# Kernel optimization log

Measured on AMD Instinct MI355X. Metric: run time of the kernel, lower is better.

The kernel has to match this reference:

```python
import jax, jax.numpy as jnp
import numpy as np

N_POINTS = 1048576
N_LEVELS = 16
F = 2
BASE_RES = 16
FINEST_RES = 512
LOG2_HASH = 19
SIZES = [2 ** min(i + 1, LOG2_HASH) for i in range(N_LEVELS)]  # per-level table rows (powers of 2)
OFFS = np.concatenate([[0], np.cumsum(SIZES)]).astype(np.int64)  # static row offsets into packed table
TOTAL_ROWS = int(OFFS[-1])  # 131070
# hash primes from the torch module; uint32 wraparound matches int64 low-bit behavior
# because each table size is a power of two <= 2^19 < 2^32, so h % 2^k == low k bits.
P0, P1, P2, P3 = np.uint32(1), np.uint32(2654435761), np.uint32(29675113), np.uint32(123456789)
CORNERS = np.array([[0,0,0],[1,0,0],[0,1,0],[1,1,0],
                    [0,0,1],[1,0,1],[0,1,1],[1,1,1]], dtype=np.uint32)  # torch stacking order


def setup_inputs() -> dict:
    key = jax.random.key(0)
    k1, k2 = jax.random.split(key)
    coords = jax.random.uniform(k1, (N_POINTS, 3), dtype=jnp.float32, minval=-1.0, maxval=1.0)
    hash_init_scale = 0.001
    table = jax.random.uniform(k2, (TOTAL_ROWS, F), dtype=jnp.float32,
                               minval=-hash_init_scale, maxval=hash_init_scale)
    return {"coords": coords, "table": table}


def _encode(coords, table):
    corners = jnp.asarray(CORNERS)  # [8,3] uint32
    outs = []
    for level in range(N_LEVELS):
        res = min(BASE_RES * (2 ** level), FINEST_RES)
        cs = (coords + 1.0) * res           # [N,3]
        cf = jnp.floor(cs)
        frac = cs - cf                      # [N,3]
        base = cf.astype(jnp.uint32)        # coords >= -1 so floor >= 0
        c = base[None, :, :] + corners[:, None, :]   # [8,N,3]
        x, y, z = c[..., 0], c[..., 1], c[..., 2]
        h = x * P0
        h = h * P1 + y
        h = h * P2 + z
        h = h * P3
        h = (h & jnp.uint32(SIZES[level] - 1)).astype(jnp.int32)  # mod power-of-2 table size
        feats = table[int(OFFS[level]) + h]          # [8,N,F] gather
        tx = frac[..., 0:1]; ty = frac[..., 1:2]; tz = frac[..., 2:3]
        f = (feats[0] * (1 - tx) * (1 - ty) * (1 - tz)
             + feats[1] * tx * (1 - ty) * (1 - tz)
             + feats[2] * (1 - tx) * ty * (1 - tz)
             + feats[3] * tx * ty * (1 - tz)
             + feats[4] * (1 - tx) * (1 - ty) * tz
             + feats[5] * tx * (1 - ty) * tz
             + feats[6] * (1 - tx) * ty * tz
             + feats[7] * tx * ty * tz)              # [N,F]
        outs.append(f)
    return jnp.concatenate(outs, axis=-1)            # [N, N_LEVELS*F]


def reference(coords, table):
    return _encode(coords, table)
```

## Files before the change

kernel.cpp:

```cpp
#include <hip/hip_runtime.h>
#include <hip/hip_fp16.h>


#define N_POINTS 1048576
#define BLOCK 1024
#define NBLOCKS 512
#define ITERS 16
#define STAGED_ROWS 16382
#define LDS_BYTES 65536

__device__ __forceinline__ float2 ldsRow(const unsigned* __restrict__ lds, unsigned idx) {
    unsigned u = lds[idx];
    __half2 h = *(__half2*)&u;
    return __half22float2(h);
}

__global__ __launch_bounds__(BLOCK) void ngp_encode_kernel(
    const float* __restrict__ coords,
    const float* __restrict__ table,
    float* __restrict__ out)
{
    extern __shared__ unsigned lds_tb[];

    {
        const float4* __restrict__ t4 = (const float4*)table;
        uint2* __restrict__ l2 = (uint2*)lds_tb;
        const int n = STAGED_ROWS / 2;
        for (int r = threadIdx.x; r < n; r += BLOCK) {
            float4 v = t4[r];
            __half2 a = __floats2half2_rn(v.x, v.y);
            __half2 b = __floats2half2_rn(v.z, v.w);
            uint2 u;
            u.x = *(unsigned*)&a;
            u.y = *(unsigned*)&b;
            l2[r] = u;
        }
    }
    __syncthreads();

    constexpr unsigned P1 = 2654435761u, P2 = 29675113u, P3 = 123456789u;
    constexpr unsigned HA = P1 * P2 * P3;
    constexpr unsigned HB = P2 * P3;
    constexpr unsigned HC = P3;
    const unsigned D[8] = {0u, HA, HB, HA + HB, HC, HA + HC, HB + HC, HA + HB + HC};

    const float2* __restrict__ tb = (const float2*)table;
    float4* __restrict__ out4 = (float4*)out;

    const int q = threadIdx.x & 7;

    for (int it = 0; it < ITERS; ++it) {
        const int t = (blockIdx.x * ITERS + it) * BLOCK + threadIdx.x;
        const int p = t >> 3;

        const float px = coords[3 * p + 0];
        const float py = coords[3 * p + 1];
        const float pz = coords[3 * p + 2];

        float4 result;
        float* rf = (float*)&result;

#pragma unroll
        for (int e = 0; e < 2; ++e) {
            const int l = 2 * q + e;
            const float fres = (l < 5) ? (float)(16 << l) : 512.0f;

            const float csx = (px + 1.0f) * fres;
            const float csy = (py + 1.0f) * fres;
            const float csz = (pz + 1.0f) * fres;
            const float cfx = floorf(csx), cfy = floorf(csy), cfz = floorf(csz);
            const float tx = csx - cfx, ty = csy - cfy, tz = csz - cfz;
            const unsigned h000 = (unsigned)cfx * HA + (unsigned)cfy * HB + (unsigned)cfz * HC;

            const float ux = 1.0f - tx, uy = 1.0f - ty, uz = 1.0f - tz;
            const float w[8] = {ux*uy*uz, tx*uy*uz, ux*ty*uz, tx*ty*uz,
                                ux*uy*tz, tx*uy*tz, ux*ty*tz, tx*ty*tz};

            const unsigned mask = (2u << l) - 1u;
            const unsigned off  = (2u << l) - 2u;

            float o0 = 0.0f, o1 = 0.0f;
            if (l <= 12) {
#pragma unroll
                for (int c = 0; c < 8; ++c) {
                    float2 f = ldsRow(lds_tb, off + ((h000 + D[c]) & mask));
                    o0 += f.x * w[c];
                    o1 += f.y * w[c];
                }
            } else {
#pragma unroll
                for (int c = 0; c < 8; ++c) {
                    float2 f = tb[off + ((h000 + D[c]) & mask)];
                    o0 += f.x * w[c];
                    o1 += f.y * w[c];
                }
            }
            rf[2 * e + 0] = o0;
            rf[2 * e + 1] = o1;
        }

        out4[t] = result;
    }
}

extern "C" void kernel_launch(void* const* d_in, const int* in_sizes, int n_in,
                              void* d_out, int out_size, void* d_ws, size_t ws_size,
                              hipStream_t stream) {
    const float* coords = (const float*)d_in[0];
    const float* table  = (const float*)d_in[1];
    float* out = (float*)d_out;

    hipFuncSetAttribute((const void*)ngp_encode_kernel,
                        hipFuncAttributeMaxDynamicSharedMemorySize,
                        LDS_BYTES);

    ngp_encode_kernel<<<NBLOCKS, BLOCK, LDS_BYTES, stream>>>(coords, table, out);
}
```

Baseline: 245.0 us.

## Map hash levels per wavefront, share 512-res hashing, transpose output through LDS

Each wavefront now handles one level pair for 64 points, instead of each lane handling a different level pair. This makes the LDS-versus-global branch uniform across the wavefront and removes divergence between the two paths. For levels that are both at 512 resolution, the floor, weight and hash work is computed once and reused for both levels. Results are transposed through an XOR-swizzled LDS buffer so global stores stay coalesced, at the cost of two block barriers per iteration. The staged half-precision table is halved so level 12 now reads from global memory, trading more global gathers for lower LDS use per block.

```diff
diff --git a/kernel.cpp b/kernel.cpp
--- a/kernel.cpp
+++ b/kernel.cpp
@@ -6,27 +6,56 @@
 #define BLOCK 1024
 #define NBLOCKS 512
 #define ITERS 16
-#define STAGED_ROWS 16382
-#define LDS_BYTES 65536
+#define STAGED_ROWS 8190
+#define TBL_LDS_BYTES 32768
+#define LDS_BYTES (TBL_LDS_BYTES + 128 * 8 * 16)
 
-__device__ __forceinline__ float2 ldsRow(const unsigned* __restrict__ lds, unsigned idx) {
+__device__ __forceinline__ float2 ldsRow(const unsigned* lds, unsigned idx) {
     unsigned u = lds[idx];
     __half2 h = *(__half2*)&u;
     return __half22float2(h);
 }
+
+#define PREP(FRES, HARR, WARR) \
+    unsigned HARR[8]; float WARR[8]; { \
+        const float csx = (px + 1.0f) * (FRES); \
+        const float csy = (py + 1.0f) * (FRES); \
+        const float csz = (pz + 1.0f) * (FRES); \
+        const float cfx = floorf(csx), cfy = floorf(csy), cfz = floorf(csz); \
+        const float tx = csx - cfx, ty = csy - cfy, tz = csz - cfz; \
+        const unsigned hh = (unsigned)cfx * HA + (unsigned)cfy * HB + (unsigned)cfz * HC; \
+        const float ux = 1.0f - tx, uy = 1.0f - ty, uz = 1.0f - tz; \
+        WARR[0] = ux*uy*uz; WARR[1] = tx*uy*uz; WARR[2] = ux*ty*uz; WARR[3] = tx*ty*uz; \
+        WARR[4] = ux*uy*tz; WARR[5] = tx*uy*tz; WARR[6] = ux*ty*tz; WARR[7] = tx*ty*tz; \
+        HARR[0] = hh;           HARR[1] = hh + HA;           \
+        HARR[2] = hh + HB;      HARR[3] = hh + HA + HB;      \
+        HARR[4] = hh + HC;      HARR[5] = hh + HA + HC;      \
+        HARR[6] = hh + HB + HC; HARR[7] = hh + HA + HB + HC; \
+    }
+
+#define GATHER_LDS(HARR, WARR, MASK, OFF, O0, O1) \
+    { _Pragma("unroll") for (int c = 0; c < 8; ++c) { \
+        float2 f = ldsRow(lds_tb, (OFF) + ((HARR[c]) & (MASK))); \
+        (O0) += f.x * WARR[c]; (O1) += f.y * WARR[c]; } }
+
+#define GATHER_GBL(HARR, WARR, MASK, OFF, O0, O1) \
+    { _Pragma("unroll") for (int c = 0; c < 8; ++c) { \
+        float2 f = tb[(OFF) + ((HARR[c]) & (MASK))]; \
+        (O0) += f.x * WARR[c]; (O1) += f.y * WARR[c]; } }
 
 __global__ __launch_bounds__(BLOCK) void ngp_encode_kernel(
     const float* __restrict__ coords,
     const float* __restrict__ table,
     float* __restrict__ out)
 {
-    extern __shared__ unsigned lds_tb[];
+    extern __shared__ unsigned char lds_raw[];
+    unsigned* lds_tb = (unsigned*)lds_raw;
+    float4* lds_out  = (float4*)(lds_raw + TBL_LDS_BYTES);
 
     {
         const float4* __restrict__ t4 = (const float4*)table;
         uint2* __restrict__ l2 = (uint2*)lds_tb;
-        const int n = STAGED_ROWS / 2;
-        for (int r = threadIdx.x; r < n; r += BLOCK) {
+        for (int r = threadIdx.x; r < STAGED_ROWS / 2; r += BLOCK) {
             float4 v = t4[r];
             __half2 a = __floats2half2_rn(v.x, v.y);
             __half2 b = __floats2half2_rn(v.z, v.w);
@@ -42,64 +71,60 @@
     constexpr unsigned HA = P1 * P2 * P3;
     constexpr unsigned HB = P2 * P3;
     constexpr unsigned HC = P3;
-    const unsigned D[8] = {0u, HA, HB, HA + HB, HC, HA + HC, HB + HC, HA + HB + HC};
 
     const float2* __restrict__ tb = (const float2*)table;
     float4* __restrict__ out4 = (float4*)out;
 
-    const int q = threadIdx.x & 7;
+    const int wv   = __builtin_amdgcn_readfirstlane((int)(threadIdx.x >> 6));
+    const int q    = wv & 7;
+    const int g    = wv >> 3;
+    const int lane = threadIdx.x & 63;
+    const int pl   = g * 64 + lane;
+
+    const int l0 = 2 * q;
+    const unsigned mask0 = (2u << l0) - 1u, off0 = mask0 - 1u;
+    const unsigned mask1 = (4u << l0) - 1u, off1 = mask1 - 1u;
 
     for (int it = 0; it < ITERS; ++it) {
-        const int t = (blockIdx.x * ITERS + it) * BLOCK + threadIdx.x;
-        const int p = t >> 3;
+        const int pbase = blockIdx.x * (ITERS * 128) + it * 128;
+        const int p = pbase + pl;
 
         const float px = coords[3 * p + 0];
         const float py = coords[3 * p + 1];
         const float pz = coords[3 * p + 2];
 
-        float4 result;
-        float* rf = (float*)&result;
+        float o00 = 0.0f, o01 = 0.0f, o10 = 0.0f, o11 = 0.0f;
 
-#pragma unroll
-        for (int e = 0; e < 2; ++e) {
-            const int l = 2 * q + e;
-            const float fres = (l < 5) ? (float)(16 << l) : 512.0f;
-
-            const float csx = (px + 1.0f) * fres;
-            const float csy = (py + 1.0f) * fres;
-            const float csz = (pz + 1.0f) * fres;
-            const float cfx = floorf(csx), cfy = floorf(csy), cfz = floorf(csz);
-            const float tx = csx - cfx, ty = csy - cfy, tz = csz - cfz;
-            const unsigned h000 = (unsigned)cfx * HA + (unsigned)cfy * HB + (unsigned)cfz * HC;
-
-            const float ux = 1.0f - tx, uy = 1.0f - ty, uz = 1.0f - tz;
-            const float w[8] = {ux*uy*uz, tx*uy*uz, ux*ty*uz, tx*ty*uz,
-                                ux*uy*tz, tx*uy*tz, ux*ty*tz, tx*ty*tz};
-
-            const unsigned mask = (2u << l) - 1u;
-            const unsigned off  = (2u << l) - 2u;
-
-            float o0 = 0.0f, o1 = 0.0f;
-            if (l <= 12) {
-#pragma unroll
-                for (int c = 0; c < 8; ++c) {
-                    float2 f = ldsRow(lds_tb, off + ((h000 + D[c]) & mask));
-                    o0 += f.x * w[c];
-                    o1 += f.y * w[c];
-                }
-            } else {
-#pragma unroll
-                for (int c = 0; c < 8; ++c) {
-                    float2 f = tb[off + ((h000 + D[c]) & mask)];
-                    o0 += f.x * w[c];
-                    o1 += f.y * w[c];
-                }
+        if (q >= 6) {
+            PREP(512.0f, hc, wc)
+            GATHER_GBL(hc, wc, mask0, off0, o00, o01)
+            GATHER_GBL(hc, wc, mask1, off1, o10, o11)
+        } else if (q >= 3) {
+            PREP(512.0f, hc, wc)
+            GATHER_LDS(hc, wc, mask0, off0, o00, o01)
+            GATHER_LDS(hc, wc, mask1, off1, o10, o11)
+        } else {
+            const float fres0 = (float)(16 << l0);
+            const float fres1 = (float)(32 << l0);
+            {
+                PREP(fres0, hA, wA)
+                GATHER_LDS(hA, wA, mask0, off0, o00, o01)
             }
-            rf[2 * e + 0] = o0;
-            rf[2 * e + 1] = o1;
+            {
+                PREP(fres1, hB, wB)
+                GATHER_LDS(hB, wB, mask1, off1, o10, o11)
+            }
         }
 
-        out4[t] = result;
+        lds_out[pl * 8 + (q ^ (pl & 7))] = make_float4(o00, o01, o10, o11);
+        __syncthreads();
+        {
+            const int j = threadIdx.x;
+            const int lp = j >> 3, qq = j & 7;
+            float4 v = lds_out[lp * 8 + (qq ^ (lp & 7))];
+            out4[(size_t)pbase * 8 + j] = v;
+        }
+        __syncthreads();
     }
 }
 
```

Result: slower. 269.0 us (+9.8%).
